# Performance work log

Hardware: AMD Instinct MI355X
Metric: run time of the kernel (lower is better)

Reference implementation:

```python
import jax, jax.numpy as jnp
import numpy as np


def setup_inputs() -> dict:
    key = jax.random.key(0)
    ks = jax.random.split(key, 12)
    B, N, D_in, D = 64, 512, 512, 512
    inp = {
        "x": jax.random.normal(ks[0], (B, N, D_in), dtype=jnp.float32),
        "adj": jax.random.uniform(ks[1], (B, N, N), dtype=jnp.float32),
        "mask": jnp.ones((B, N, 1), dtype=jnp.float32),
        "W_enc": jax.random.normal(ks[2], (D_in, D), dtype=jnp.float32) * (1.0 / np.sqrt(D_in)),
        "b_enc": jnp.zeros((D,), dtype=jnp.float32),
        "Wz": jax.random.normal(ks[3], (D, D), dtype=jnp.float32) * (1.0 / np.sqrt(D)),
        "Uz": jax.random.normal(ks[4], (D, D), dtype=jnp.float32) * (1.0 / np.sqrt(D)),
        "bz": jnp.zeros((D,), dtype=jnp.float32),
        "Wr": jax.random.normal(ks[5], (D, D), dtype=jnp.float32) * (1.0 / np.sqrt(D)),
        "Ur": jax.random.normal(ks[6], (D, D), dtype=jnp.float32) * (1.0 / np.sqrt(D)),
        "br": jnp.zeros((D,), dtype=jnp.float32),
        "Wh": jax.random.normal(ks[7], (D, D), dtype=jnp.float32) * (1.0 / np.sqrt(D)),
        "Uh": jax.random.normal(ks[8], (D, D), dtype=jnp.float32) * (1.0 / np.sqrt(D)),
        "bh": jnp.zeros((D,), dtype=jnp.float32),
        "ba": jnp.zeros((D,), dtype=jnp.float32),
        "steps": 2,
    }
    return inp


def _gru_step(h, adj, mask, Wz, Uz, bz, Wr, Ur, br, Wh, Uh, bh, ba, act):
    # aggregated neighbor messages: [B,N,D]
    a = jnp.einsum('bnm,bmd->bnd', adj, h) + ba
    z = act(a @ Wz + h @ Uz + bz)          # update gate
    r = act(a @ Wr + h @ Ur + br)          # reset gate
    hc = jnp.tanh(a @ Wh + (r * h) @ Uh + bh)
    hc = hc * mask
    return (1.0 - z) * h + z * hc


def reference(x, adj, mask, W_enc, b_enc, Wz, Uz, bz, Wr, Ur, br, Wh, Uh, bh, ba, steps):
    act = jax.nn.relu
    h = mask * act(x @ W_enc + b_enc)      # [B,N,D]
    for _ in range(steps):
        h = _gru_step(h, adj, mask, Wz, Uz, bz, Wr, Ur, br, Wh, Uh, bh, ba, act)
    return h
```

## Files before the change

kernel.cpp:

```cpp
#include <hip/hip_runtime.h>


#define LD 512

typedef unsigned short u16;
typedef _Float16 f16;
typedef f16 f16x8 __attribute__((ext_vector_type(8)));
typedef float f32x4 __attribute__((ext_vector_type(4)));

__device__ __forceinline__ u16 f2h(float f) { f16 h = (f16)f; return *(u16*)&h; }
__device__ __forceinline__ float h2f(u16 b) { f16 h = *(f16*)&b; return (float)h; }

__device__ __forceinline__ void gload16(const void* g, void* l) {
  __builtin_amdgcn_global_load_lds(
      (const __attribute__((address_space(1))) void*)g,
      (__attribute__((address_space(3))) void*)l, 16, 0, 0);
}

__global__ void cvt_f16(const float* __restrict__ in, u16* __restrict__ out, int n4) {
  int i = blockIdx.x * blockDim.x + threadIdx.x;
  if (i >= n4) return;
  float4 v = reinterpret_cast<const float4*>(in)[i];
  ushort4 o;
  o.x = f2h(v.x); o.y = f2h(v.y); o.z = f2h(v.z); o.w = f2h(v.w);
  reinterpret_cast<ushort4*>(out)[i] = o;
}

__global__ void cvt2h(const float* __restrict__ in, u16* __restrict__ ohi,
                      u16* __restrict__ olo, int n4) {
  int i = blockIdx.x * blockDim.x + threadIdx.x;
  if (i >= n4) return;
  float4 v = reinterpret_cast<const float4*>(in)[i];
  ushort4 h, l;
  h.x = f2h(v.x); l.x = f2h(v.x - h2f(h.x));
  h.y = f2h(v.y); l.y = f2h(v.y - h2f(h.y));
  h.z = f2h(v.z); l.z = f2h(v.z - h2f(h.z));
  h.w = f2h(v.w); l.w = f2h(v.w - h2f(h.w));
  reinterpret_cast<ushort4*>(ohi)[i] = h;
  reinterpret_cast<ushort4*>(olo)[i] = l;
}

__global__ void wconv1(const float* __restrict__ in, u16* __restrict__ out, float scale) {
  __shared__ float sm[32][33];
  int tx = threadIdx.x & 31, ty = threadIdx.x >> 5;
  int k0 = blockIdx.y * 32, n0 = blockIdx.x * 32;
#pragma unroll
  for (int i = 0; i < 32; i += 8)
    sm[ty + i][tx] = in[(size_t)(k0 + ty + i) * LD + n0 + tx];
  __syncthreads();
#pragma unroll
  for (int i = 0; i < 32; i += 8)
    out[(size_t)(n0 + ty + i) * LD + k0 + tx] = f2h(sm[tx][ty + i] * scale);
}

__global__ void wconv2h(const float* __restrict__ in, u16* __restrict__ ohi,
                        u16* __restrict__ olo, float scale) {
  __shared__ float sm[32][33];
  int tx = threadIdx.x & 31, ty = threadIdx.x >> 5;
  int k0 = blockIdx.y * 32, n0 = blockIdx.x * 32;
#pragma unroll
  for (int i = 0; i < 32; i += 8)
    sm[ty + i][tx] = in[(size_t)(k0 + ty + i) * LD + n0 + tx];
  __syncthreads();
#pragma unroll
  for (int i = 0; i < 32; i += 8) {
    float v = sm[tx][ty + i] * scale;
    u16 hi = f2h(v);
    size_t o = (size_t)(n0 + ty + i) * LD + k0 + tx;
    ohi[o] = hi;
    olo[o] = f2h(v - h2f(hi));
  }
}

__global__ void transp16(const u16* __restrict__ in, u16* __restrict__ out) {
  __shared__ u16 sm[64][65];
  int b = blockIdx.z;
  int n0 = blockIdx.y * 64, d0 = blockIdx.x * 64;
  int lane = threadIdx.x & 63, grp = threadIdx.x >> 6;
  const u16* src = in + ((size_t)b * LD + n0) * LD + d0;
#pragma unroll
  for (int i = grp; i < 64; i += 4)
    sm[i][lane] = src[(size_t)i * LD + lane];
  __syncthreads();
  u16* dst = out + ((size_t)b * LD + d0) * LD + n0;
#pragma unroll
  for (int i = grp; i < 64; i += 4)
    dst[(size_t)i * LD + lane] = sm[lane][i];
}

struct Desc {
  const u16* A[6];
  const u16* B[6];
  long bsA, bsB;
  const float* bias1;
  const float* mask;
  const float* hf32;
  const u16* z16;
  float* outf;
  u16* o16;
  u16* o16b;
};

template <int MODE, int NA>
__global__ __launch_bounds__(512, 2) void gemm8(Desc d) {
  constexpr int NT = NA * 16;
  constexpr int GYB = (MODE == 1) ? 2 : 128;
  constexpr int RPB = (MODE == 1) ? 512 : 0;

  __shared__ __align__(16) u16 lds[65536];

  const int t = threadIdx.x;
  const int lane = t & 63;
  const int wid = t >> 6;
  const int wr = wid >> 2, wc = wid & 3;

  const int id = (int)blockIdx.x;
  const int swz = (id & 7) * 32 + (id >> 3);
  const int bx = swz & 1;
  const int by = (swz >> 1) % GYB;
  const size_t bz = (size_t)((swz >> 1) / GYB);

  const int p0 = t, p1 = t + 512;
  const int r0 = p0 >> 2, c0 = ((p0 & 3) ^ ((p0 >> 3) & 3)) * 8;
  const int r1 = p1 >> 2, c1 = ((p1 & 3) ^ ((p1 >> 3) & 3)) * 8;

  const int rA0 = wr * 128 + (lane & 15);
  const int rB0 = wc * 64 + (lane & 15);
  const int aoff = rA0 * 32 + (((lane >> 4) ^ ((rA0 >> 1) & 3)) * 8);
  const int boff = 8192 + rB0 * 32 + (((lane >> 4) ^ ((rB0 >> 1) & 3)) * 8);

  f32x4 acc[8][4] = {};

  const size_t rowOffA = (size_t)by * 256 * LD;
  const size_t rowOffB = (size_t)bx * 256 * LD;

  auto stageH = [&](int tt, int half) {
    const u16* Ap = d.A[tt >> 4] + bz * d.bsA + rowOffA;
    const u16* Bp = d.B[tt >> 4] + bz * d.bsB + rowOffB;
    const int kb = (tt & 15) * 32;
    u16* Lb = &lds[(tt & 3) * 16384];
    if (half == 0) {
      gload16(Ap + (size_t)r0 * LD + kb + c0, Lb + p0 * 8);
      gload16(Bp + (size_t)r0 * LD + kb + c0, Lb + 8192 + p0 * 8);
    } else {
      gload16(Ap + (size_t)r1 * LD + kb + c1, Lb + p1 * 8);
      gload16(Bp + (size_t)r1 * LD + kb + c1, Lb + 8192 + p1 * 8);
    }
  };

  stageH(0, 0); stageH(0, 1);
  stageH(1, 0); stageH(1, 1);
  stageH(2, 0); stageH(2, 1);
  asm volatile("s_waitcnt vmcnt(8)" ::: "memory");
  __builtin_amdgcn_s_barrier();

  for (int tt = 0; tt < NT; ++tt) {
    const u16* L = &lds[(tt & 3) * 16384];
    const bool st = (tt + 3) < NT;
    f16x8 bfr[4], af[4];
    if (st) stageH(tt + 3, 0);
#pragma unroll
    for (int j = 0; j < 4; ++j) bfr[j] = *(const f16x8*)&L[boff + j * 512];
#pragma unroll
    for (int i = 0; i < 4; ++i) af[i] = *(const f16x8*)&L[aoff + i * 512];
    __builtin_amdgcn_s_setprio(1);
#pragma unroll
    for (int i = 0; i < 4; ++i)
#pragma unroll
      for (int j = 0; j < 4; ++j)
        acc[i][j] = __builtin_amdgcn_mfma_f32_16x16x32_f16(af[i], bfr[j], acc[i][j], 0, 0, 0);
    __builtin_amdgcn_s_setprio(0);
    if (st) stageH(tt + 3, 1);
#pragma unroll
    for (int i = 0; i < 4; ++i) af[i] = *(const f16x8*)&L[aoff + (i + 4) * 512];
    __builtin_amdgcn_s_setprio(1);
#pragma unroll
    for (int i = 0; i < 4; ++i)
#pragma unroll
      for (int j = 0; j < 4; ++j)
        acc[i + 4][j] =
            __builtin_amdgcn_mfma_f32_16x16x32_f16(af[i], bfr[j], acc[i + 4][j], 0, 0, 0);
    __builtin_amdgcn_s_setprio(0);
    asm volatile("s_waitcnt lgkmcnt(0)" ::: "memory");
    if (tt + 4 < NT) {
      asm volatile("s_waitcnt vmcnt(8)" ::: "memory");
    } else {
      asm volatile("s_waitcnt vmcnt(0)" ::: "memory");
    }
    __builtin_amdgcn_s_barrier();
  }

  const float S4 = 0.0625f;
  const float S12 = 2.44140625e-4f;
  const int rowBase = (int)bz * RPB + by * 256 + wr * 128 + (lane >> 4) * 4;
  const int colBase = bx * 256 + wc * 64 + (lane & 15);
#pragma unroll
  for (int i = 0; i < 8; ++i) {
#pragma unroll
    for (int j = 0; j < 4; ++j) {
      const int col = colBase + j * 16;
      const float bv = d.bias1[col];
#pragma unroll
      for (int r = 0; r < 4; ++r) {
        const int row = rowBase + i * 16 + r;
        const size_t idx = (size_t)row * LD + col;
        const float a = acc[i][j][r];
        if (MODE == 0) {
          float v = fmaxf(a + bv, 0.0f) * d.mask[row];
          d.outf[idx] = v;
          d.o16[idx] = f2h(v * S4);
        } else if (MODE == 1) {
          float v = a + bv * S4;
          u16 hi = f2h(v);
          d.o16[idx] = hi;
          d.o16b[idx] = f2h(v - h2f(hi));
        } else if (MODE == 2) {
          float v = fmaxf(a + bv, 0.0f);
          d.o16[idx] = f2h(v * S4);
        } else if (MODE == 3) {
          float v = fmaxf(a + bv, 0.0f) * d.hf32[idx];
          u16 hi = f2h(v * S12);
          d.o16[idx] = hi;
          float rec = h2f(hi) * 4096.0f;
          d.o16b[idx] = f2h((v - rec) * S12);
        } else {
          float hc = tanhf(a + bv) * d.mask[row];
          float z = 16.0f * h2f(d.z16[idx]);
          float h = d.hf32[idx];
          float hn = (1.0f - z) * h + z * hc;
          d.outf[idx] = hn;
          d.o16[idx] = f2h(hn * S4);
        }
      }
    }
  }
}

extern "C" void kernel_launch(void* const* d_in, const int* in_sizes, int n_in,
                              void* d_out, int out_size, void* d_ws, size_t ws_size,
                              hipStream_t stream) {
  const float* x    = (const float*)d_in[0];
  const float* adj  = (const float*)d_in[1];
  const float* mask = (const float*)d_in[2];
  const float* Wenc = (const float*)d_in[3];
  const float* benc = (const float*)d_in[4];
  const float* Wz   = (const float*)d_in[5];
  const float* Uz   = (const float*)d_in[6];
  const float* bz_  = (const float*)d_in[7];
  const float* Wr   = (const float*)d_in[8];
  const float* Ur   = (const float*)d_in[9];
  const float* br_  = (const float*)d_in[10];
  const float* Wh   = (const float*)d_in[11];
  const float* Uh   = (const float*)d_in[12];
  const float* bh_  = (const float*)d_in[13];
  const float* ba_  = (const float*)d_in[14];

  float* hf = (float*)d_out;

  const size_t SZ  = (size_t)64 * 512 * 512 * sizeof(u16);
  const size_t WSZ = (size_t)LD * LD * sizeof(u16);
  const size_t NEED = 7 * SZ + 11 * WSZ;
  if (ws_size < NEED) return;

  char* p = (char*)d_ws;
  u16* adj16 = (u16*)p; p += SZ;
  u16* h16   = (u16*)p; p += SZ;
  u16* a_hi  = (u16*)p; p += SZ;
  u16* a_lo  = (u16*)p; p += SZ;
  u16* zht   = (u16*)p; p += SZ;
  u16* rh_hi = (u16*)p; p += SZ;
  u16* rh_lo = (u16*)p; p += SZ;
  u16* w     = (u16*)p;
  u16* We_h = w + 0 * LD * LD;  u16* We_l = w + 1 * LD * LD;
  u16* Wz1  = w + 2 * LD * LD;
  u16* Uz1  = w + 3 * LD * LD;
  u16* Wr_h = w + 4 * LD * LD;  u16* Wr_l = w + 5 * LD * LD;
  u16* Ur1  = w + 6 * LD * LD;
  u16* Wh_h = w + 7 * LD * LD;  u16* Wh_l = w + 8 * LD * LD;
  u16* Uh_h = w + 9 * LD * LD;  u16* Uh_l = w + 10 * LD * LD;
  u16* x_hi = a_hi;
  u16* x_lo = a_lo;

  const int NELT = 64 * 512 * 512;
  cvt2h<<<NELT / 4 / 256, 256, 0, stream>>>(x, x_hi, x_lo, NELT / 4);
  cvt_f16<<<NELT / 4 / 256, 256, 0, stream>>>(adj, adj16, NELT / 4);

  dim3 wg(16, 16);
  wconv2h<<<wg, 256, 0, stream>>>(Wenc, We_h, We_l, 1.0f);
  wconv1<<<wg, 256, 0, stream>>>(Wz, Wz1, 16.0f);
  wconv1<<<wg, 256, 0, stream>>>(Uz, Uz1, 16.0f);
  wconv2h<<<wg, 256, 0, stream>>>(Wr, Wr_h, Wr_l, 16.0f);
  wconv1<<<wg, 256, 0, stream>>>(Ur, Ur1, 16.0f);
  wconv2h<<<wg, 256, 0, stream>>>(Wh, Wh_h, Wh_l, 16.0f);
  wconv2h<<<wg, 256, 0, stream>>>(Uh, Uh_h, Uh_l, 4096.0f);

  const long NN = (long)LD * LD;

  {
    Desc d{};
    d.A[0] = x_hi; d.B[0] = We_h;
    d.A[1] = x_lo; d.B[1] = We_h;
    d.A[2] = x_hi; d.B[2] = We_l;
    d.bias1 = benc; d.mask = mask; d.outf = hf; d.o16 = h16;
    gemm8<0, 3><<<256, 512, 0, stream>>>(d);
  }

  for (int s = 0; s < 2; ++s) {
    transp16<<<dim3(8, 8, 64), 256, 0, stream>>>(h16, zht);
    {
      Desc d{};
      d.A[0] = adj16; d.B[0] = zht; d.bsA = NN; d.bsB = NN;
      d.bias1 = ba_; d.o16 = a_hi; d.o16b = a_lo;
      gemm8<1, 1><<<256, 512, 0, stream>>>(d);
    }
    {
      Desc d{};
      d.A[0] = a_hi; d.B[0] = Wz1;
      d.A[1] = h16;  d.B[1] = Uz1;
      d.bias1 = bz_; d.o16 = zht;
      gemm8<2, 2><<<256, 512, 0, stream>>>(d);
    }
    {
      Desc d{};
      d.A[0] = a_hi; d.B[0] = Wr_h;
      d.A[1] = a_hi; d.B[1] = Wr_l;
      d.A[2] = a_lo; d.B[2] = Wr_h;
      d.A[3] = h16;  d.B[3] = Ur1;
      d.bias1 = br_; d.hf32 = hf; d.o16 = rh_hi; d.o16b = rh_lo;
      gemm8<3, 4><<<256, 512, 0, stream>>>(d);
    }
    if (s == 0) {
      Desc d{};
      d.A[0] = a_hi;  d.B[0] = Wh_h;
      d.A[1] = a_hi;  d.B[1] = Wh_l;
      d.A[2] = a_lo;  d.B[2] = Wh_h;
      d.A[3] = rh_hi; d.B[3] = Uh_h;
      d.A[4] = rh_hi; d.B[4] = Uh_l;
      d.A[5] = rh_lo; d.B[5] = Uh_h;
      d.bias1 = bh_; d.mask = mask; d.hf32 = hf; d.z16 = zht;
      d.outf = hf; d.o16 = h16;
      gemm8<4, 6><<<256, 512, 0, stream>>>(d);
    } else {
      Desc d{};
      d.A[0] = a_hi;  d.B[0] = Wh_h;
      d.A[1] = rh_hi; d.B[1] = Uh_h;
      d.bias1 = bh_; d.mask = mask; d.hf32 = hf; d.z16 = zht;
      d.outf = hf; d.o16 = h16;
      gemm8<4, 2><<<256, 512, 0, stream>>>(d);
    }
  }
}
```

Measured before the change: 778.8 us.

## Switch GEMM main loop to K=64 double-buffered tiles with phased staging

```diff
diff --git a/kernel.cpp b/kernel.cpp
--- a/kernel.cpp
+++ b/kernel.cpp
@@ -2,6 +2,7 @@
 
 
 #define LD 512
+#define CFENCE asm volatile("" ::: "memory")
 
 typedef unsigned short u16;
 typedef _Float16 f16;
@@ -103,7 +104,7 @@
 
 template <int MODE, int NA>
 __global__ __launch_bounds__(512, 2) void gemm8(Desc d) {
-  constexpr int NT = NA * 16;
+  constexpr int NT = NA * 8;
   constexpr int GYB = (MODE == 1) ? 2 : 128;
   constexpr int RPB = (MODE == 1) ? 512 : 0;
 
@@ -120,74 +121,90 @@
   const int by = (swz >> 1) % GYB;
   const size_t bz = (size_t)((swz >> 1) / GYB);
 
-  const int p0 = t, p1 = t + 512;
-  const int r0 = p0 >> 2, c0 = ((p0 & 3) ^ ((p0 >> 3) & 3)) * 8;
-  const int r1 = p1 >> 2, c1 = ((p1 & 3) ^ ((p1 >> 3) & 3)) * 8;
-
-  const int rA0 = wr * 128 + (lane & 15);
-  const int rB0 = wc * 64 + (lane & 15);
-  const int aoff = rA0 * 32 + (((lane >> 4) ^ ((rA0 >> 1) & 3)) * 8);
-  const int boff = 8192 + rB0 * 32 + (((lane >> 4) ^ ((rB0 >> 1) & 3)) * 8);
+  const int lsw = lane & 7;
+  const int lk = lane >> 4;
+  const int rowA = wr * 128 + (lane & 15);
+  const int rowB = wc * 64 + (lane & 15);
+  int aofs[2], bofs[2];
+#pragma unroll
+  for (int ks = 0; ks < 2; ++ks) {
+    aofs[ks] = rowA * 64 + (((ks * 4 + lk) ^ lsw) * 8);
+    bofs[ks] = 16384 + rowB * 64 + (((ks * 4 + lk) ^ lsw) * 8);
+  }
 
   f32x4 acc[8][4] = {};
+  f16x8 bfr[8];
 
   const size_t rowOffA = (size_t)by * 256 * LD;
   const size_t rowOffB = (size_t)bx * 256 * LD;
 
-  auto stageH = [&](int tt, int half) {
-    const u16* Ap = d.A[tt >> 4] + bz * d.bsA + rowOffA;
-    const u16* Bp = d.B[tt >> 4] + bz * d.bsB + rowOffB;
-    const int kb = (tt & 15) * 32;
-    u16* Lb = &lds[(tt & 3) * 16384];
-    if (half == 0) {
-      gload16(Ap + (size_t)r0 * LD + kb + c0, Lb + p0 * 8);
-      gload16(Bp + (size_t)r0 * LD + kb + c0, Lb + 8192 + p0 * 8);
+  auto stagePair = [&](int tt, int ph) {
+    const u16* Ap = d.A[tt >> 3] + bz * d.bsA + rowOffA;
+    const u16* Bp = d.B[tt >> 3] + bz * d.bsB + rowOffB;
+    const int kb = (tt & 7) * 64;
+    u16* Lb = &lds[(tt & 1) * 32768];
+    if (ph < 2) {
+      const int i0 = t, i1 = t + 512;
+      const int r0 = 128 * ph + (i0 >> 3), c0 = i0 & 7;
+      const int r1 = 128 * ph + (i1 >> 3), c1 = i1 & 7;
+      gload16(Bp + (size_t)r0 * LD + kb + ((c0 ^ (r0 & 7)) * 8),
+              Lb + 16384 + r0 * 64 + c0 * 8);
+      gload16(Bp + (size_t)r1 * LD + kb + ((c1 ^ (r1 & 7)) * 8),
+              Lb + 16384 + r1 * 64 + c1 * 8);
     } else {
-      gload16(Ap + (size_t)r1 * LD + kb + c1, Lb + p1 * 8);
-      gload16(Bp + (size_t)r1 * LD + kb + c1, Lb + 8192 + p1 * 8);
+      const int s0 = 2 * (ph - 2), s1 = s0 + 1;
+      const int rr = (t >> 8) * 128 + ((t >> 3) & 31), cc = t & 7;
+      const int r0 = 32 * s0 + rr, r1 = 32 * s1 + rr;
+      gload16(Ap + (size_t)r0 * LD + kb + ((cc ^ (r0 & 7)) * 8),
+              Lb + r0 * 64 + cc * 8);
+      gload16(Ap + (size_t)r1 * LD + kb + ((cc ^ (r1 & 7)) * 8),
+              Lb + r1 * 64 + cc * 8);
     }
   };
 
-  stageH(0, 0); stageH(0, 1);
-  stageH(1, 0); stageH(1, 1);
-  stageH(2, 0); stageH(2, 1);
-  asm volatile("s_waitcnt vmcnt(8)" ::: "memory");
+  stagePair(0, 0); stagePair(0, 1); stagePair(0, 2); stagePair(0, 3);
+  asm volatile("s_waitcnt vmcnt(2)" ::: "memory");
   __builtin_amdgcn_s_barrier();
 
   for (int tt = 0; tt < NT; ++tt) {
-    const u16* L = &lds[(tt & 3) * 16384];
-    const bool st = (tt + 3) < NT;
-    f16x8 bfr[4], af[4];
-    if (st) stageH(tt + 3, 0);
-#pragma unroll
-    for (int j = 0; j < 4; ++j) bfr[j] = *(const f16x8*)&L[boff + j * 512];
-#pragma unroll
-    for (int i = 0; i < 4; ++i) af[i] = *(const f16x8*)&L[aoff + i * 512];
-    __builtin_amdgcn_s_setprio(1);
-#pragma unroll
-    for (int i = 0; i < 4; ++i)
-#pragma unroll
-      for (int j = 0; j < 4; ++j)
-        acc[i][j] = __builtin_amdgcn_mfma_f32_16x16x32_f16(af[i], bfr[j], acc[i][j], 0, 0, 0);
-    __builtin_amdgcn_s_setprio(0);
-    if (st) stageH(tt + 3, 1);
-#pragma unroll
-    for (int i = 0; i < 4; ++i) af[i] = *(const f16x8*)&L[aoff + (i + 4) * 512];
-    __builtin_amdgcn_s_setprio(1);
-#pragma unroll
-    for (int i = 0; i < 4; ++i)
-#pragma unroll
-      for (int j = 0; j < 4; ++j)
-        acc[i + 4][j] =
-            __builtin_amdgcn_mfma_f32_16x16x32_f16(af[i], bfr[j], acc[i + 4][j], 0, 0, 0);
-    __builtin_amdgcn_s_setprio(0);
-    asm volatile("s_waitcnt lgkmcnt(0)" ::: "memory");
-    if (tt + 4 < NT) {
-      asm volatile("s_waitcnt vmcnt(8)" ::: "memory");
-    } else {
-      asm volatile("s_waitcnt vmcnt(0)" ::: "memory");
-    }
-    __builtin_amdgcn_s_barrier();
+    const u16* L = &lds[(tt & 1) * 32768];
+    const bool st = (tt + 1) < NT;
+#pragma unroll
+    for (int p = 0; p < 4; ++p) {
+      if (p == 0) {
+#pragma unroll
+        for (int j = 0; j < 4; ++j)
+#pragma unroll
+          for (int ks = 0; ks < 2; ++ks)
+            bfr[j * 2 + ks] = *(const f16x8*)&L[bofs[ks] + j * 1024];
+      }
+      f16x8 af[2][2];
+#pragma unroll
+      for (int di = 0; di < 2; ++di)
+#pragma unroll
+        for (int ks = 0; ks < 2; ++ks)
+          af[di][ks] = *(const f16x8*)&L[aofs[ks] + (2 * p + di) * 1024];
+      if (st) stagePair(tt + 1, p);
+      __builtin_amdgcn_s_setprio(1);
+#pragma unroll
+      for (int di = 0; di < 2; ++di)
+#pragma unroll
+        for (int j = 0; j < 4; ++j) {
+          acc[2 * p + di][j] = __builtin_amdgcn_mfma_f32_16x16x32_f16(
+              af[di][0], bfr[j * 2 + 0], acc[2 * p + di][j], 0, 0, 0);
+          acc[2 * p + di][j] = __builtin_amdgcn_mfma_f32_16x16x32_f16(
+              af[di][1], bfr[j * 2 + 1], acc[2 * p + di][j], 0, 0, 0);
+        }
+      __builtin_amdgcn_s_setprio(0);
+      if (p == 1) {
+        if (st) asm volatile("s_waitcnt vmcnt(4)" ::: "memory");
+        else    asm volatile("s_waitcnt vmcnt(0)" ::: "memory");
+      } else if (p == 3) {
+        if (st) asm volatile("s_waitcnt vmcnt(2)" ::: "memory");
+      }
+      CFENCE;
+      __builtin_amdgcn_s_barrier();
+    }
   }
 
   const float S4 = 0.0625f;
```

Measured after the change: 736.2 us. 1.06x faster.
